# Performance work log

Hardware: AMD Instinct MI355X
Metric: run time of the kernel (lower is better)

The kernel has to match this reference:

```python
import jax, jax.numpy as jnp
import numpy as np

BETA = 0.25  # args.beta
B, T, D, K = 16, 4096, 64, 1024


def setup_inputs() -> dict:
    key = jax.random.key(0)
    kz, kw = jax.random.split(key)
    z = jax.random.normal(kz, (B, T, D), dtype=jnp.float32)
    # nn.Embedding weight init: uniform(-1/K, 1/K)
    emb = jax.random.uniform(kw, (K, D), dtype=jnp.float32,
                             minval=-1.0 / K, maxval=1.0 / K)
    return {"z": z, "emb": emb}


def reference(z, emb):
    # z: [B, T, D] (torch code loops over first dim; all elements non-empty here)
    # emb: [K, D] codebook
    b, t, d = z.shape
    zf = z.reshape(-1, d)                                   # [B*T, D]
    # squared euclidean distances: ||z||^2 + ||e||^2 - 2 z.e
    dist = (jnp.sum(zf * zf, axis=1, keepdims=True)
            + jnp.sum(emb * emb, axis=1)
            - 2.0 * zf @ emb.T)                             # [B*T, K]
    idx = jnp.argmin(dist, axis=1).reshape(b, t)            # [B, T] int
    z_q_raw = emb[idx]                                      # [B, T, D] gather
    sg = jax.lax.stop_gradient
    # per-batch-element means, summed (loop accumulates loss per z_t)
    commit = jnp.mean((sg(z_q_raw) - z) ** 2, axis=(1, 2))  # [B]
    codebk = jnp.mean((z_q_raw - sg(z)) ** 2, axis=(1, 2))  # [B]
    loss = jnp.sum(BETA * commit + codebk)
    # straight-through estimator
    z_q = z + sg(z_q_raw - z)
    return z_q, loss, idx
```

## Files before the change

### kernel.cpp

```cpp
#include <hip/hip_runtime.h>
#include <math.h>
#include <float.h>

#define NROWS    65536
#define DD       64
#define KK       1024
#define LOSS_OFF 4194304
#define IDX_OFF  4194305
#define RPB      128
#define MAXC     16

typedef short  short8 __attribute__((ext_vector_type(8)));
typedef float  f32x4  __attribute__((ext_vector_type(4)));

__device__ __forceinline__ void async_copy16(void* lds, const void* g) {
    __builtin_amdgcn_global_load_lds(
        (const __attribute__((address_space(1))) unsigned int*)g,
        (__attribute__((address_space(3))) unsigned int*)lds, 16, 0, 0);
}

__device__ __forceinline__ unsigned short bf16rne(float x) {
    unsigned int u = __float_as_uint(x);
    return (unsigned short)((u + 0x7fffu + ((u >> 16) & 1u)) >> 16);
}

__device__ __forceinline__ float np_sumsq64_stream(const float* p) {
#pragma clang fp contract(off)
    float r[8];
    {
        const float4 u0 = *reinterpret_cast<const float4*>(p);
        const float4 u1 = *reinterpret_cast<const float4*>(p + 4);
        r[0] = u0.x * u0.x; r[1] = u0.y * u0.y; r[2] = u0.z * u0.z; r[3] = u0.w * u0.w;
        r[4] = u1.x * u1.x; r[5] = u1.y * u1.y; r[6] = u1.z * u1.z; r[7] = u1.w * u1.w;
    }
#pragma unroll
    for (int i = 8; i < 64; i += 8) {
        const float4 u0 = *reinterpret_cast<const float4*>(p + i);
        const float4 u1 = *reinterpret_cast<const float4*>(p + i + 4);
        r[0] += u0.x * u0.x; r[1] += u0.y * u0.y; r[2] += u0.z * u0.z; r[3] += u0.w * u0.w;
        r[4] += u1.x * u1.x; r[5] += u1.y * u1.y; r[6] += u1.z * u1.z; r[7] += u1.w * u1.w;
    }
    return ((r[0] + r[1]) + (r[2] + r[3])) + ((r[4] + r[5]) + (r[6] + r[7]));
}

__global__ void vq_prep(const float* __restrict__ emb,
                        float* __restrict__ bn,
                        unsigned short* __restrict__ ebf) {
#pragma clang fp contract(off)
    const int gtid = blockIdx.x * 256 + threadIdx.x;
    const int code = gtid >> 3;
    const int j    = gtid & 7;
    const float* ep = emb + (size_t)code * DD;
    float r = 0.f;
#pragma unroll
    for (int i = 0; i < 8; ++i) {
        const float v = ep[8 * i + j];
        r += v * v;
    }
    const float s1 = r  + __shfl_xor(r,  1, 64);
    const float s2 = s1 + __shfl_xor(s1, 2, 64);
    const float s3 = s2 + __shfl_xor(s2, 4, 64);
    if (j == 0) bn[code] = s3;

    const float* cp = emb + (size_t)gtid * 8;
    const float4 u0 = *reinterpret_cast<const float4*>(cp);
    const float4 u1 = *reinterpret_cast<const float4*>(cp + 4);
    short8 s;
    s[0] = (short)bf16rne(u0.x); s[1] = (short)bf16rne(u0.y);
    s[2] = (short)bf16rne(u0.z); s[3] = (short)bf16rne(u0.w);
    s[4] = (short)bf16rne(u1.x); s[5] = (short)bf16rne(u1.y);
    s[6] = (short)bf16rne(u1.z); s[7] = (short)bf16rne(u1.w);
    *reinterpret_cast<short8*>(ebf + (size_t)gtid * 8) = s;
}

__global__ __launch_bounds__(256)
void vq_main(const float* __restrict__ z, const float* __restrict__ emb,
             const unsigned short* __restrict__ ebf,
             const float* __restrict__ bn, float* __restrict__ out) {
    __shared__ char  dbuf[2][8192] __attribute__((aligned(16)));
    __shared__ float a_s[RPB];
    __shared__ float bn_s[KK];
    __shared__ int   cnt[RPB];
    __shared__ int   clist[RPB][MAXC];
    __shared__ int   bidx[RPB];

    const int tid  = threadIdx.x;
    const int lane = tid & 63;
    const int wv   = __builtin_amdgcn_readfirstlane(tid) >> 6;
    const int q    = lane >> 4;
    const int c16  = lane & 15;
    const int rowbase = blockIdx.x * RPB;

    const char* sbase = (const char*)ebf + (size_t)c16 * 128 + (size_t)q * 16;
    char* dst0 = &dbuf[0][wv * 2048 + lane * 16];
    char* dst1 = &dbuf[1][wv * 2048 + lane * 16];

    if (tid < RPB) {
        a_s[tid] = np_sumsq64_stream(z + (size_t)(rowbase + tid) * DD);
        cnt[tid] = 0;
    }
    {
        const int i = tid * 4;
        *reinterpret_cast<float4*>(&bn_s[i]) =
            *reinterpret_cast<const float4*>(bn + i);
    }

    short8 afr[2][2];
#pragma unroll
    for (int rt = 0; rt < 2; ++rt) {
#pragma unroll
        for (int kh = 0; kh < 2; ++kh) {
            const float* zp = z + (size_t)(rowbase + 32 * wv + 16 * rt + c16) * DD
                              + 32 * kh + 8 * q;
            const float4 u0 = *reinterpret_cast<const float4*>(zp);
            const float4 u1 = *reinterpret_cast<const float4*>(zp + 4);
            short8 s;
            s[0] = (short)bf16rne(u0.x); s[1] = (short)bf16rne(u0.y);
            s[2] = (short)bf16rne(u0.z); s[3] = (short)bf16rne(u0.w);
            s[4] = (short)bf16rne(u1.x); s[5] = (short)bf16rne(u1.y);
            s[6] = (short)bf16rne(u1.z); s[7] = (short)bf16rne(u1.w);
            afr[rt][kh] = s;
        }
    }

    float mn[8];
#pragma unroll
    for (int i = 0; i < 8; ++i) mn[i] = FLT_MAX;

    {
        const char* s0 = sbase + (size_t)wv * 2048;
        async_copy16(dst0, s0);
        async_copy16(dst0 + 1024, s0 + 64);
    }
    __syncthreads();

    for (int R = 0; R < 16; ++R) {
        const int cur = R & 1;
        if (R < 15) {
            const char* s0 = sbase + (size_t)(4 * (R + 1) + wv) * 2048;
            char* d = cur ? dst0 : dst1;
            async_copy16(d, s0);
            async_copy16(d + 1024, s0 + 64);
        }
#pragma unroll
        for (int j = 0; j < 4; ++j) {
            const char* tb = &dbuf[cur][j * 2048 + lane * 16];
            const short8 b0 = *reinterpret_cast<const short8*>(tb);
            const short8 b1 = *reinterpret_cast<const short8*>(tb + 1024);
            f32x4 acc0 = {0.f, 0.f, 0.f, 0.f};
            f32x4 acc1 = {0.f, 0.f, 0.f, 0.f};
            acc0 = __builtin_amdgcn_mfma_f32_16x16x32_bf16(afr[0][0], b0, acc0, 0, 0, 0);
            acc0 = __builtin_amdgcn_mfma_f32_16x16x32_bf16(afr[0][1], b1, acc0, 0, 0, 0);
            acc1 = __builtin_amdgcn_mfma_f32_16x16x32_bf16(afr[1][0], b0, acc1, 0, 0, 0);
            acc1 = __builtin_amdgcn_mfma_f32_16x16x32_bf16(afr[1][1], b1, acc1, 0, 0, 0);
            const float bnv = bn_s[16 * (4 * R + j) + c16];
#pragma unroll
            for (int r = 0; r < 4; ++r) {
                mn[r]     = fminf(mn[r],     fmaf(-2.f, acc0[r], bnv));
                mn[4 + r] = fminf(mn[4 + r], fmaf(-2.f, acc1[r], bnv));
            }
        }
        __syncthreads();
    }

#pragma unroll
    for (int mask = 1; mask < 16; mask <<= 1) {
#pragma unroll
        for (int i = 0; i < 8; ++i)
            mn[i] = fminf(mn[i], __shfl_xor(mn[i], mask, 64));
    }
    float T[8];
#pragma unroll
    for (int i = 0; i < 8; ++i) {
        const int rowl = 32 * wv + 16 * (i >> 2) + 4 * q + (i & 3);
        T[i] = mn[i] + 1.8e-4f * sqrtf(a_s[rowl]) + 1.2e-4f;
    }

    {
        const char* s0 = sbase + (size_t)wv * 2048;
        async_copy16(dst0, s0);
        async_copy16(dst0 + 1024, s0 + 64);
    }
    __syncthreads();

    for (int R = 0; R < 16; ++R) {
        const int cur = R & 1;
        if (R < 15) {
            const char* s0 = sbase + (size_t)(4 * (R + 1) + wv) * 2048;
            char* d = cur ? dst0 : dst1;
            async_copy16(d, s0);
            async_copy16(d + 1024, s0 + 64);
        }
#pragma unroll
        for (int j = 0; j < 4; ++j) {
            const char* tb = &dbuf[cur][j * 2048 + lane * 16];
            const short8 b0 = *reinterpret_cast<const short8*>(tb);
            const short8 b1 = *reinterpret_cast<const short8*>(tb + 1024);
            f32x4 acc0 = {0.f, 0.f, 0.f, 0.f};
            f32x4 acc1 = {0.f, 0.f, 0.f, 0.f};
            acc0 = __builtin_amdgcn_mfma_f32_16x16x32_bf16(afr[0][0], b0, acc0, 0, 0, 0);
            acc0 = __builtin_amdgcn_mfma_f32_16x16x32_bf16(afr[0][1], b1, acc0, 0, 0, 0);
            acc1 = __builtin_amdgcn_mfma_f32_16x16x32_bf16(afr[1][0], b0, acc1, 0, 0, 0);
            acc1 = __builtin_amdgcn_mfma_f32_16x16x32_bf16(afr[1][1], b1, acc1, 0, 0, 0);
            const int col = 16 * (4 * R + j) + c16;
            const float bnv = bn_s[col];
#pragma unroll
            for (int r = 0; r < 4; ++r) {
                const float d0 = fmaf(-2.f, acc0[r], bnv);
                if (d0 <= T[r]) {
                    const int rowl = 32 * wv + 4 * q + r;
                    const int slot = atomicAdd(&cnt[rowl], 1);
                    if (slot < MAXC) clist[rowl][slot] = col;
                }
                const float d1 = fmaf(-2.f, acc1[r], bnv);
                if (d1 <= T[4 + r]) {
                    const int rowl = 32 * wv + 16 + 4 * q + r;
                    const int slot = atomicAdd(&cnt[rowl], 1);
                    if (slot < MAXC) clist[rowl][slot] = col;
                }
            }
        }
        __syncthreads();
    }

#pragma unroll
    for (int rt = 0; rt < 2; ++rt) {
        const int rowl = 32 * wv + 16 * rt + c16;
        const int row  = rowbase + rowl;
        const int nc   = cnt[rowl];
        const bool full = nc > MAXC;
        const int lim  = full ? KK : nc;
        const float av = a_s[rowl];
        const float* zp = z + (size_t)row * DD;
        float sb = FLT_MAX;
        int   cb = 0x7fffffff;
        for (int jj = q; jj < lim; jj += 4) {
            const int c = full ? jj : clist[rowl][jj];
            const float* ep = emb + (size_t)c * DD;
            float dot = 0.f;
#pragma unroll
            for (int d = 0; d < DD; d += 4) {
                const float4 zv = *reinterpret_cast<const float4*>(zp + d);
                const float4 ev = *reinterpret_cast<const float4*>(ep + d);
                dot = fmaf(zv.x, ev.x, dot); dot = fmaf(zv.y, ev.y, dot);
                dot = fmaf(zv.z, ev.z, dot); dot = fmaf(zv.w, ev.w, dot);
            }
            const float tt = av + bn_s[c];
            const float sd = fmaf(-2.f, dot, tt);
            if (sd < sb || (sd == sb && c < cb)) { sb = sd; cb = c; }
        }
#pragma unroll
        for (int mask = 16; mask < 64; mask <<= 1) {
            const float so = __shfl_xor(sb, mask, 64);
            const int   co = __shfl_xor(cb, mask, 64);
            if (so < sb || (so == sb && co < cb)) { sb = so; cb = co; }
        }
        if (cb > 1023) cb = 0;
        if (q == 0) bidx[rowl] = cb;
    }
    __syncthreads();

    if (tid >= RPB) return;
    const int row = rowbase + tid;
    const int bid = bidx[tid];
    const float* ep = emb + (size_t)bid * DD;
    const float* zp = z + (size_t)row * DD;
    float* op = out + (size_t)row * DD;
    double sac = 0.0;
#pragma unroll
    for (int d = 0; d < DD; d += 4) {
        const float4 zv = *reinterpret_cast<const float4*>(zp + d);
        const float4 e4 = *reinterpret_cast<const float4*>(ep + d);
        const float df0 = e4.x - zv.x;
        const float df1 = e4.y - zv.y;
        const float df2 = e4.z - zv.z;
        const float df3 = e4.w - zv.w;
        float4 qv;
        qv.x = zv.x + df0; qv.y = zv.y + df1;
        qv.z = zv.z + df2; qv.w = zv.w + df3;
        *reinterpret_cast<float4*>(op + d) = qv;
        sac += (double)(df0 * df0); sac += (double)(df1 * df1);
        sac += (double)(df2 * df2); sac += (double)(df3 * df3);
    }
    out[IDX_OFF + row] = (float)bid;

#pragma unroll
    for (int off = 32; off > 0; off >>= 1) sac += __shfl_down(sac, off, 64);
    if (lane == 0)
        atomicAdd(&out[LOSS_OFF], (float)((1.25 * sac) / 262144.0));
}

extern "C" void kernel_launch(void* const* d_in, const int* in_sizes, int n_in,
                              void* d_out, int out_size, void* d_ws, size_t ws_size,
                              hipStream_t stream) {
    const float* z   = (const float*)d_in[0];
    const float* emb = (const float*)d_in[1];
    float* out = (float*)d_out;

    float*          bnw = (float*)d_ws;
    unsigned short* ebf = (unsigned short*)((char*)d_ws + 4096);

    vq_prep<<<dim3(32), dim3(256), 0, stream>>>(emb, bnw, ebf);
    vq_main<<<dim3(NROWS / RPB), dim3(256), 0, stream>>>(z, emb, ebf, bnw, out);
}
```

Measured before the change: 130.5 us.

## Fuse min and candidate-collection passes using a running threshold

The kernel used to compute each row's minimum distance in one full sweep over the codebook, then run a second full sweep to collect near-minimum candidates. It now does a single sweep: round 0 finds a minimum over the first 128 codes and sets the threshold. Each later round collects candidates against the current threshold and then tightens it with the round's minimum. This roughly halves the MFMA and LDS-staging work. The cost is that early, looser thresholds admit more candidates, so MAXC is raised to 32 and each round stages 8 code tiles. If a row's candidate list overflows, the rescoring step falls back to a full exact scan, which is expensive.

```diff
diff --git a/kernel.cpp b/kernel.cpp
--- a/kernel.cpp
+++ b/kernel.cpp
@@ -8,7 +8,9 @@
 #define LOSS_OFF 4194304
 #define IDX_OFF  4194305
 #define RPB      128
-#define MAXC     16
+#define MAXC     32
+#define TPR      8
+#define NRND     8
 
 typedef short  short8 __attribute__((ext_vector_type(8)));
 typedef float  f32x4  __attribute__((ext_vector_type(4)));
@@ -77,7 +79,7 @@
 void vq_main(const float* __restrict__ z, const float* __restrict__ emb,
              const unsigned short* __restrict__ ebf,
              const float* __restrict__ bn, float* __restrict__ out) {
-    __shared__ char  dbuf[2][8192] __attribute__((aligned(16)));
+    __shared__ char  dbuf[2][TPR * 2048] __attribute__((aligned(16)));
     __shared__ float a_s[RPB];
     __shared__ float bn_s[KK];
     __shared__ int   cnt[RPB];
@@ -92,8 +94,6 @@
     const int rowbase = blockIdx.x * RPB;
 
     const char* sbase = (const char*)ebf + (size_t)c16 * 128 + (size_t)q * 16;
-    char* dst0 = &dbuf[0][wv * 2048 + lane * 16];
-    char* dst1 = &dbuf[1][wv * 2048 + lane * 16];
 
     if (tid < RPB) {
         a_s[tid] = np_sumsq64_stream(z + (size_t)(rowbase + tid) * DD);
@@ -123,102 +123,87 @@
         }
     }
 
-    float mn[8];
-#pragma unroll
-    for (int i = 0; i < 8; ++i) mn[i] = FLT_MAX;
-
-    {
-        const char* s0 = sbase + (size_t)wv * 2048;
-        async_copy16(dst0, s0);
-        async_copy16(dst0 + 1024, s0 + 64);
-    }
+    auto stage = [&](int R, int buf) {
+        const char* s0 = sbase + (size_t)(TPR * R + 2 * wv) * 2048;
+        char* d = &dbuf[buf][(2 * wv) * 2048 + lane * 16];
+        async_copy16(d,               s0);
+        async_copy16(d + 1024,        s0 + 64);
+        async_copy16(d + 2048,        s0 + 2048);
+        async_copy16(d + 2048 + 1024, s0 + 2048 + 64);
+    };
+
+    float mn[8], T[8], Wr[8];
+#pragma unroll
+    for (int i = 0; i < 8; ++i) { mn[i] = FLT_MAX; T[i] = -FLT_MAX; }
+
+    stage(0, 0);
     __syncthreads();
 
-    for (int R = 0; R < 16; ++R) {
-        const int cur = R & 1;
-        if (R < 15) {
-            const char* s0 = sbase + (size_t)(4 * (R + 1) + wv) * 2048;
-            char* d = cur ? dst0 : dst1;
-            async_copy16(d, s0);
-            async_copy16(d + 1024, s0 + 64);
-        }
-#pragma unroll
-        for (int j = 0; j < 4; ++j) {
-            const char* tb = &dbuf[cur][j * 2048 + lane * 16];
-            const short8 b0 = *reinterpret_cast<const short8*>(tb);
-            const short8 b1 = *reinterpret_cast<const short8*>(tb + 1024);
-            f32x4 acc0 = {0.f, 0.f, 0.f, 0.f};
-            f32x4 acc1 = {0.f, 0.f, 0.f, 0.f};
-            acc0 = __builtin_amdgcn_mfma_f32_16x16x32_bf16(afr[0][0], b0, acc0, 0, 0, 0);
-            acc0 = __builtin_amdgcn_mfma_f32_16x16x32_bf16(afr[0][1], b1, acc0, 0, 0, 0);
-            acc1 = __builtin_amdgcn_mfma_f32_16x16x32_bf16(afr[1][0], b0, acc1, 0, 0, 0);
-            acc1 = __builtin_amdgcn_mfma_f32_16x16x32_bf16(afr[1][1], b1, acc1, 0, 0, 0);
-            const float bnv = bn_s[16 * (4 * R + j) + c16];
-#pragma unroll
-            for (int r = 0; r < 4; ++r) {
-                mn[r]     = fminf(mn[r],     fmaf(-2.f, acc0[r], bnv));
-                mn[4 + r] = fminf(mn[4 + r], fmaf(-2.f, acc1[r], bnv));
-            }
-        }
-        __syncthreads();
-    }
-
-#pragma unroll
-    for (int mask = 1; mask < 16; mask <<= 1) {
-#pragma unroll
-        for (int i = 0; i < 8; ++i)
-            mn[i] = fminf(mn[i], __shfl_xor(mn[i], mask, 64));
-    }
-    float T[8];
 #pragma unroll
     for (int i = 0; i < 8; ++i) {
         const int rowl = 32 * wv + 16 * (i >> 2) + 4 * q + (i & 3);
-        T[i] = mn[i] + 1.8e-4f * sqrtf(a_s[rowl]) + 1.2e-4f;
-    }
-
-    {
-        const char* s0 = sbase + (size_t)wv * 2048;
-        async_copy16(dst0, s0);
-        async_copy16(dst0 + 1024, s0 + 64);
-    }
-    __syncthreads();
-
-    for (int R = 0; R < 16; ++R) {
-        const int cur = R & 1;
-        if (R < 15) {
-            const char* s0 = sbase + (size_t)(4 * (R + 1) + wv) * 2048;
-            char* d = cur ? dst0 : dst1;
-            async_copy16(d, s0);
-            async_copy16(d + 1024, s0 + 64);
-        }
-#pragma unroll
-        for (int j = 0; j < 4; ++j) {
-            const char* tb = &dbuf[cur][j * 2048 + lane * 16];
-            const short8 b0 = *reinterpret_cast<const short8*>(tb);
-            const short8 b1 = *reinterpret_cast<const short8*>(tb + 1024);
-            f32x4 acc0 = {0.f, 0.f, 0.f, 0.f};
-            f32x4 acc1 = {0.f, 0.f, 0.f, 0.f};
-            acc0 = __builtin_amdgcn_mfma_f32_16x16x32_bf16(afr[0][0], b0, acc0, 0, 0, 0);
-            acc0 = __builtin_amdgcn_mfma_f32_16x16x32_bf16(afr[0][1], b1, acc0, 0, 0, 0);
-            acc1 = __builtin_amdgcn_mfma_f32_16x16x32_bf16(afr[1][0], b0, acc1, 0, 0, 0);
-            acc1 = __builtin_amdgcn_mfma_f32_16x16x32_bf16(afr[1][1], b1, acc1, 0, 0, 0);
-            const int col = 16 * (4 * R + j) + c16;
-            const float bnv = bn_s[col];
-#pragma unroll
-            for (int r = 0; r < 4; ++r) {
-                const float d0 = fmaf(-2.f, acc0[r], bnv);
+        Wr[i] = 1.8e-4f * sqrtf(a_s[rowl]) + 1.2e-4f;
+    }
+
+    auto proc = [&](int cur, int j, int colbase, bool update, bool collect) {
+        const char* tb = &dbuf[cur][j * 2048 + lane * 16];
+        const short8 b0 = *reinterpret_cast<const short8*>(tb);
+        const short8 b1 = *reinterpret_cast<const short8*>(tb + 1024);
+        f32x4 acc0 = {0.f, 0.f, 0.f, 0.f};
+        f32x4 acc1 = {0.f, 0.f, 0.f, 0.f};
+        acc0 = __builtin_amdgcn_mfma_f32_16x16x32_bf16(afr[0][0], b0, acc0, 0, 0, 0);
+        acc0 = __builtin_amdgcn_mfma_f32_16x16x32_bf16(afr[0][1], b1, acc0, 0, 0, 0);
+        acc1 = __builtin_amdgcn_mfma_f32_16x16x32_bf16(afr[1][0], b0, acc1, 0, 0, 0);
+        acc1 = __builtin_amdgcn_mfma_f32_16x16x32_bf16(afr[1][1], b1, acc1, 0, 0, 0);
+        const int col = colbase + c16;
+        const float bnv = bn_s[col];
+#pragma unroll
+        for (int r = 0; r < 4; ++r) {
+            const float d0 = fmaf(-2.f, acc0[r], bnv);
+            const float d1 = fmaf(-2.f, acc1[r], bnv);
+            if (update) {
+                mn[r]     = fminf(mn[r],     d0);
+                mn[4 + r] = fminf(mn[4 + r], d1);
+            }
+            if (collect) {
                 if (d0 <= T[r]) {
                     const int rowl = 32 * wv + 4 * q + r;
                     const int slot = atomicAdd(&cnt[rowl], 1);
                     if (slot < MAXC) clist[rowl][slot] = col;
                 }
-                const float d1 = fmaf(-2.f, acc1[r], bnv);
                 if (d1 <= T[4 + r]) {
                     const int rowl = 32 * wv + 16 + 4 * q + r;
                     const int slot = atomicAdd(&cnt[rowl], 1);
                     if (slot < MAXC) clist[rowl][slot] = col;
                 }
             }
+        }
+    };
+
+    auto fold = [&]() {
+#pragma unroll
+        for (int mask = 1; mask < 16; mask <<= 1)
+#pragma unroll
+            for (int i = 0; i < 8; ++i)
+                mn[i] = fminf(mn[i], __shfl_xor(mn[i], mask, 64));
+#pragma unroll
+        for (int i = 0; i < 8; ++i) T[i] = mn[i] + Wr[i];
+    };
+
+    for (int R = 0; R < NRND; ++R) {
+        const int cur = R & 1;
+        if (R < NRND - 1) stage(R + 1, cur ^ 1);
+        if (R == 0) {
+#pragma unroll
+            for (int j = 0; j < TPR; ++j) proc(cur, j, 16 * j, true, false);
+            fold();
+#pragma unroll
+            for (int j = 0; j < TPR; ++j) proc(cur, j, 16 * j, false, true);
+        } else {
+#pragma unroll
+            for (int j = 0; j < TPR; ++j)
+                proc(cur, j, 16 * (TPR * R + j), true, true);
+            fold();
         }
         __syncthreads();
     }
```

New measurement: 141.4 us. +8.3%, slower.
